# Kernel tuning notes

Measured on AMD Instinct MI355X. Metric: run time of the kernel, lower is better.

The kernel has to match this reference:

```python
import jax, jax.numpy as jnp
import numpy as np

B = 256      # batch
ZD = 128     # z_dim
HIN = 128    # H_inputs
H = 512      # hidden
HT = 32      # H_t
N = 16384    # num nodes
RW = 16      # rw_len
TEMP = 1.0
P_DROP = 0.2
EPS_C = 0.1  # constraints epsilon


def setup_inputs() -> dict:
    key = jax.random.key(0)
    ks = jax.random.split(key, 20)
    def w(k, shape, fan):
        return (jax.random.normal(k, shape, jnp.float32) / np.float32(np.sqrt(fan)))
    z = lambda n: jnp.zeros((n,), jnp.float32)
    u = jax.random.uniform(ks[14], (RW, B, N), jnp.float32)
    return {
        "latent": jax.random.normal(ks[0], (B, ZD + 1), jnp.float32),
        "inputs0": jnp.zeros((B, HIN), jnp.float32),
        "Wc": w(ks[1], (ZD, ZD + 1), ZD + 1), "bc": z(ZD),
        "Ws": w(ks[2], (H, ZD), ZD), "bs": z(H),
        "Wh": w(ks[3], (H, H), H), "bh": z(H),
        "Wcc": w(ks[4], (H, H), H), "bcc": z(H),
        "W_ih": w(ks[5], (4 * H, HIN), HIN), "b_ih": z(4 * H),
        "W_hh": w(ks[6], (4 * H, H), H), "b_hh": z(4 * H),
        "W_up": w(ks[7], (N, H), H), "b_up": z(N),
        "W_down": w(ks[8], (HIN, N), N),
        "Wt_down": w(ks[9], (HT, H), H), "bt_down": z(HT),
        "Wt_pred": w(ks[10], (1, HT), HT),
        "Wt_up": w(ks[11], (HT, 1), 1), "bt_up": z(HT),
        "W_vt": w(ks[12], (HIN, HIN + HT), HIN + HT),
        "W_prob": w(ks[13], (1, HIN), HIN),
        # pre-sampled Gumbel noise per step (torch.rand -> gumbel)
        "gumbel": -jnp.log(-jnp.log(u + 1e-20) + 1e-20),
        # uniforms for dropout masks in TimeDecoder (forced train mode)
        "drop_u": jax.random.uniform(ks[15], (RW, B, HT), jnp.float32),
    }


def reference(latent, inputs0, Wc, bc, Ws, bs, Wh, bh, Wcc, bcc,
              W_ih, b_ih, W_hh, b_hh, W_up, b_up, W_down,
              Wt_down, bt_down, Wt_pred, Wt_up, bt_up, W_vt, W_prob,
              gumbel, drop_u):
    # induced=True path: compress latent, init (h, c)
    lat = jnp.tanh(latent @ Wc.T + bc)               # [B, ZD]
    s = jnp.tanh(lat @ Ws.T + bs)                    # [B, H]
    h0 = jnp.tanh(s @ Wh.T + bh)
    c0 = jnp.tanh(s @ Wcc.T + bcc)
    keep = 1.0 - P_DROP

    def step(carry, xs):
        x, h, c, last_t = carry
        g, du = xs
        # torch LSTMCell: gate order i, f, g, o
        gates = x @ W_ih.T + b_ih + h @ W_hh.T + b_hh  # [B, 4H]
        i, f, gg, o = jnp.split(gates, 4, axis=1)
        c2 = jax.nn.sigmoid(f) * c + jax.nn.sigmoid(i) * jnp.tanh(gg)
        h2 = jax.nn.sigmoid(o) * jnp.tanh(c2)
        # node logits + gumbel-softmax sample
        p = h2 @ W_up.T + b_up                         # [B, N]
        v = jax.nn.softmax((p + g) / TEMP, axis=1)
        Hg = v @ W_down.T                              # [B, HIN]
        # TimeDecoder (dropout always in train mode)
        td = jnp.tanh(h2 @ Wt_down.T + bt_down)        # [B, HT]
        td = td * (du < keep).astype(td.dtype) / keep
        t = jnp.minimum(td @ Wt_pred.T, 1.0)           # [B, 1]
        # constraints(t, last_t)
        mn = jnp.min(t)
        t = jnp.where(mn < EPS_C, t - mn, t)
        mx = jnp.max(t)
        t = jnp.where(mx > 1.0, t / mx, t)
        t = jnp.clip(t, last_t, 1.0)
        Ht = t @ Wt_up.T + bt_up                       # [B, HT]
        x2 = jnp.concatenate([Hg, Ht], axis=1) @ W_vt.T  # [B, HIN]
        return (x2, h2, c2, t), (v, t)

    last_t0 = jnp.zeros((latent.shape[0], 1), latent.dtype)
    (xf, _, _, _), (rw, ts) = jax.lax.scan(step, (inputs0, h0, c0, last_t0), (gumbel, drop_u))
    rw = jnp.transpose(rw, (1, 0, 2))   # [B, RW, N]
    ts = jnp.transpose(ts, (1, 0, 2))   # [B, RW, 1]
    prob = xf @ W_prob.T                # [B, 1]
    return rw, ts, prob
```

## Files before the change

### kernel.cpp

```cpp
#include <hip/hip_runtime.h>

typedef float  __attribute__((ext_vector_type(4))) f32x4;
typedef int    __attribute__((ext_vector_type(4))) i32x4;
typedef unsigned short u16;
typedef unsigned long long u64;

#define B    256
#define H    512
#define HIN  128
#define N    16384
#define RW   16
#define HT   32
#define KC2  672
#define RWN  262144
#define TS_OFF   67108864
#define PROB_OFF 67112960

__device__ __forceinline__ u16 f2bf(float f) {
  unsigned u = __builtin_bit_cast(unsigned, f);
  u += 0x7FFFu + ((u >> 16) & 1u);
  return (u16)(u >> 16);
}
__device__ __forceinline__ float bf2f(u16 v) {
  return __builtin_bit_cast(float, ((unsigned)v) << 16);
}
__device__ __forceinline__ float sigm(float x) { return 1.0f / (1.0f + expf(-x)); }

__device__ __forceinline__ void mfma(f32x4& d, i32x4 a, i32x4 b) {
  asm volatile("v_mfma_f32_16x16x32_bf16 %0, %1, %2, %0" : "+v"(d) : "v"(a), "v"(b));
}
__device__ __forceinline__ void mfma_n(f32x4& d, i32x4 a, i32x4 b) {
  asm volatile("s_nop 1\n\tv_mfma_f32_16x16x32_bf16 %0, %1, %2, %0" : "+v"(d) : "v"(a), "v"(b));
}
__device__ __forceinline__ void fence_acc(f32x4& v) {
  asm volatile("s_nop 7\n\ts_nop 7" : "+v"(v));
}

__global__ __launch_bounds__(256) void k_prep(
    const float* __restrict__ W_up, const float* __restrict__ W_down,
    const float* __restrict__ W_hh, const float* __restrict__ Wt_down,
    const float* __restrict__ b_ih, const float* __restrict__ b_hh,
    const float* __restrict__ Wh, const float* __restrict__ Wcc,
    u16* __restrict__ Wup_b, u16* __restrict__ Wdn_b, u16* __restrict__ Wfull,
    u16* __restrict__ Wtd_b, u16* __restrict__ Whc_b,
    float* __restrict__ bcomb, float* __restrict__ tstep, float* __restrict__ rowLs)
{
  const int idx0 = blockIdx.x * 256 + threadIdx.x;
  const int stride = gridDim.x * 256;
  for (int i = idx0; i < N * H; i += stride) Wup_b[i] = f2bf(W_up[i]);
  for (int i = idx0; i < HIN * N; i += stride) Wdn_b[i] = f2bf(W_down[i]);
  for (int i = idx0; i < 4 * H * H; i += stride) {
    int j = i >> 9, k = i & 511;
    Wfull[j * KC2 + 160 + k] = f2bf(W_hh[i]);
  }
  for (int i = idx0; i < HT * H; i += stride) Wtd_b[i] = f2bf(Wt_down[i]);
  for (int i = idx0; i < 2 * H * H; i += stride) {
    int j = i >> 9, k = i & 511;
    Whc_b[i] = f2bf(j < H ? Wh[j * H + k] : Wcc[(j - H) * H + k]);
  }
  for (int i = idx0; i < 4 * H; i += stride) bcomb[i] = b_ih[i] + b_hh[i];
  for (int i = idx0; i < B; i += stride) tstep[i] = 0.0f;
  for (int i = idx0; i < 16 * B; i += stride) rowLs[i] = 0.0f;
}

__global__ __launch_bounds__(256) void k_fold(
    const float* __restrict__ W_ih, const float* __restrict__ W_vt,
    const float* __restrict__ inputs0, const float* __restrict__ W_prob,
    u16* __restrict__ Wfull, float* __restrict__ g0add, float* __restrict__ wpc)
{
  int idx = blockIdx.x * 256 + threadIdx.x;
  if (idx < 2048 * 160) {
    int j = idx / 160, m = idx - j * 160;
    float a = 0.0f;
    for (int c = 0; c < HIN; ++c) a += W_ih[j * HIN + c] * W_vt[c * 160 + m];
    Wfull[j * KC2 + m] = f2bf(a);
  } else if (idx < 2048 * 160 + 256 * 2048) {
    int i2 = idx - 2048 * 160;
    int b = i2 >> 11, j = i2 & 2047;
    float a = 0.0f;
    for (int k = 0; k < HIN; ++k) a += inputs0[b * HIN + k] * W_ih[j * HIN + k];
    g0add[i2] = a;
  } else if (idx < 2048 * 160 + 256 * 2048 + 160) {
    int m = idx - (2048 * 160 + 256 * 2048);
    float a = 0.0f;
    for (int k = 0; k < HIN; ++k) a += W_prob[k] * W_vt[k * 160 + m];
    wpc[m] = a;
  }
}

__global__ __launch_bounds__(256) void k_lat(
    const float* __restrict__ latent, const float* __restrict__ Wc,
    const float* __restrict__ bc, float* __restrict__ latbuf)
{
  int idx = blockIdx.x * 256 + threadIdx.x;
  int b = idx >> 7, i = idx & 127;
  float acc = bc[i];
  for (int k = 0; k < 129; ++k) acc += latent[b * 129 + k] * Wc[i * 129 + k];
  latbuf[idx] = tanhf(acc);
}

__global__ __launch_bounds__(256) void k_sinit(
    const float* __restrict__ latbuf, const float* __restrict__ Ws,
    const float* __restrict__ bs, u16* __restrict__ sinit_b)
{
  int idx = blockIdx.x * 256 + threadIdx.x;
  int b = idx >> 9, j = idx & 511;
  float acc = bs[j];
  for (int k = 0; k < HIN; ++k) acc += latbuf[b * HIN + k] * Ws[j * HIN + k];
  sinit_b[idx] = f2bf(tanhf(acc));
}

__global__ __launch_bounds__(256) void k_h0c0m(
    const u16* __restrict__ sinit_b, const u16* __restrict__ Whc_b,
    const float* __restrict__ bh, const float* __restrict__ bcc,
    float* __restrict__ cbuf, u16* __restrict__ h0out)
{
  const int rb = blockIdx.x >> 6, cb = blockIdx.x & 63;
  const int wave = threadIdx.x >> 6, lane = threadIdx.x & 63;
  const int lr = lane & 15, lk = lane >> 4;
  const int m0 = rb * 16, col0 = cb * 16;
  const u16* ab = sinit_b + (m0 + lr) * H + wave * 128 + 8 * lk;
  const u16* bb = Whc_b + (col0 + lr) * H + wave * 128 + 8 * lk;
  f32x4 acc[2] = {};
  mfma_n(acc[0], *(const i32x4*)(ab),      *(const i32x4*)(bb));
  mfma_n(acc[1], *(const i32x4*)(ab + 32), *(const i32x4*)(bb + 32));
  mfma(acc[0], *(const i32x4*)(ab + 64), *(const i32x4*)(bb + 64));
  mfma(acc[1], *(const i32x4*)(ab + 96), *(const i32x4*)(bb + 96));
  fence_acc(acc[0]); fence_acc(acc[1]);
  __shared__ float q[4][16][17];
  #pragma unroll
  for (int rr = 0; rr < 4; ++rr)
    q[wave][4 * lk + rr][lr] = acc[0][rr] + acc[1][rr];
  __syncthreads();
  const int r2 = threadIdx.x >> 4, jj = threadIdx.x & 15;
  float s = q[0][r2][jj] + q[1][r2][jj] + q[2][r2][jj] + q[3][r2][jj];
  int col = col0 + jj;
  if (col < H) h0out[(m0 + r2) * H + col] = f2bf(tanhf(s + bh[col]));
  else         cbuf[(m0 + r2) * H + col - H] = tanhf(s + bcc[col - H]);
}

__global__ __launch_bounds__(256) void k_lstm2(
    const u16* __restrict__ hprev, u16* __restrict__ hcur,
    const u16* __restrict__ Wfull, const float* __restrict__ bcomb,
    float* __restrict__ cbuf, const float* __restrict__ g0,
    const float* __restrict__ HgfPrev, float* __restrict__ HgfNext,
    const float* __restrict__ rowLs, const float* __restrict__ t0buf,
    float* __restrict__ tstep, const float* __restrict__ Wt_up,
    const float* __restrict__ bt_up, float* __restrict__ out,
    const u16* __restrict__ ebp, int r)
{
  const int blk = blockIdx.x, tid = threadIdx.x;
  const int wave = tid >> 6, lane = tid & 63;
  const int lr = lane & 15, lk = lane >> 4;
  const int rb = blk & 15, cb = blk >> 4;
  const int m0 = rb * 16, j0 = cb * 16;
  const float* rowLprev = rowLs + (r - 1) * B;

  __shared__ u16 aT[16][168];
  __shared__ float q[4][16][17];
  __shared__ float redS[8];
  __shared__ float tl[256];

  if (blk < 128) HgfNext[blk * 256 + tid] = 0.0f;

  float tv = 0.0f;
  if (r > 0) {
    tv = t0buf[tid];
    float v = tv;
    #pragma unroll
    for (int off = 1; off < 64; off <<= 1) v = fminf(v, __shfl_xor(v, off));
    if (lane == 0) redS[wave] = v;
  }
  __syncthreads();
  if (r > 0) {
    float mn = fminf(fminf(redS[0], redS[1]), fminf(redS[2], redS[3]));
    if (mn < 0.1f) tv -= mn;
    float v = tv;
    #pragma unroll
    for (int off = 1; off < 64; off <<= 1) v = fmaxf(v, __shfl_xor(v, off));
    if (lane == 0) redS[4 + wave] = v;
  }
  __syncthreads();
  if (r > 0) {
    float mx = fmaxf(fmaxf(redS[4], redS[5]), fmaxf(redS[6], redS[7]));
    if (mx > 1.0f) tv /= mx;
    tv = fminf(fmaxf(tv, tstep[(r - 1) * B + tid]), 1.0f);
    if (blk == 0) {
      tstep[r * B + tid] = tv;
      out[TS_OFF + tid * RW + (r - 1)] = tv;
    }
  }
  tl[tid] = tv;

  {
    const int row = tid >> 4, c8 = (tid & 15) * 8;
    if (r > 0) {
      const float* hp = HgfPrev + (m0 + row) * HIN + c8;
      f32x4 x0 = *(const f32x4*)hp;
      f32x4 x1 = *(const f32x4*)(hp + 4);
      float R = 1.0f / rowLprev[m0 + row];
      aT[row][c8 + 0] = f2bf(x0[0] * R); aT[row][c8 + 1] = f2bf(x0[1] * R);
      aT[row][c8 + 2] = f2bf(x0[2] * R); aT[row][c8 + 3] = f2bf(x0[3] * R);
      aT[row][c8 + 4] = f2bf(x1[0] * R); aT[row][c8 + 5] = f2bf(x1[1] * R);
      aT[row][c8 + 6] = f2bf(x1[2] * R); aT[row][c8 + 7] = f2bf(x1[3] * R);
    } else {
      #pragma unroll
      for (int e = 0; e < 8; ++e) aT[row][c8 + e] = 0;
    }
  }

  __syncthreads();
  for (int i2 = tid; i2 < 512; i2 += 256) {
    int row = i2 >> 5, j = i2 & 31;
    aT[row][128 + j] = (r > 0) ? f2bf(tl[m0 + row] * Wt_up[j] + bt_up[j]) : (u16)0;
  }

  if (r > 0) {
    #pragma unroll
    for (int uu = 0; uu < 8; ++uu) {
      int flat = (blk * 2048 + uu * 256 + tid) * 4;
      int row = flat >> 14;
      float Rv = 1.0f / rowLprev[row];
      u64 ev = *(const u64*)(ebp + flat);
      f32x4 o;
      o[0] = bf2f((u16)ev) * Rv;
      o[1] = bf2f((u16)(ev >> 16)) * Rv;
      o[2] = bf2f((u16)(ev >> 32)) * Rv;
      o[3] = bf2f((u16)(ev >> 48)) * Rv;
      *(f32x4*)(out + (size_t)row * RWN + (size_t)(r - 1) * N + (flat & (N - 1))) = o;
    }
  }
  __syncthreads();

  const int gcol = wave * H + j0 + lr;
  f32x4 acc[2] = {};
  const u16* brow = Wfull + (size_t)gcol * KC2 + 8 * lk;
  const u16* aL   = &aT[lr][8 * lk];
  const u16* arow = hprev + (m0 + lr) * H + 8 * lk;
  mfma_n(acc[0], *(const i32x4*)(aL),       *(const i32x4*)(brow));
  mfma_n(acc[1], *(const i32x4*)(aL + 32),  *(const i32x4*)(brow + 32));
  mfma(acc[0], *(const i32x4*)(aL + 64),  *(const i32x4*)(brow + 64));
  mfma(acc[1], *(const i32x4*)(aL + 96),  *(const i32x4*)(brow + 96));
  mfma(acc[0], *(const i32x4*)(aL + 128), *(const i32x4*)(brow + 128));
  #pragma unroll 4
  for (int i = 5; i < 21; ++i) {
    int kk = i * 32;
    mfma(acc[i & 1], *(const i32x4*)(arow + kk - 160), *(const i32x4*)(brow + kk));
  }
  fence_acc(acc[0]); fence_acc(acc[1]);
  float bias = bcomb[gcol];
  #pragma unroll
  for (int rr = 0; rr < 4; ++rr)
    q[wave][4 * lk + rr][lr] = acc[0][rr] + acc[1][rr] + bias;
  __syncthreads();
  const int r2 = tid >> 4, jj = tid & 15;
  const int b = m0 + r2, j = j0 + jj;
  float gi = q[0][r2][jj], gf = q[1][r2][jj], gg = q[2][r2][jj], go = q[3][r2][jj];
  if (r == 0) {
    const float* gp = g0 + b * 2048 + j;
    gi += gp[0]; gf += gp[512]; gg += gp[1024]; go += gp[1536];
  }
  float c  = cbuf[b * H + j];
  float c2 = sigm(gf) * c + sigm(gi) * tanhf(gg);
  float h2 = sigm(go) * tanhf(c2);
  cbuf[b * H + j] = c2;
  hcur[b * H + j] = f2bf(h2);
}

__global__ __launch_bounds__(256) void k_pgemm2(
    const u16* __restrict__ hb, const u16* __restrict__ Wup,
    const float* __restrict__ b_up, const float* __restrict__ gum,
    u16* __restrict__ eb, float* __restrict__ rowL,
    float* __restrict__ HgfAcc, const u16* __restrict__ Wdn,
    const u16* __restrict__ Wtd, const float* __restrict__ bt_down,
    const float* __restrict__ Wt_pred, const float* __restrict__ du,
    float* __restrict__ t0)
{
  const int rb = blockIdx.x >> 7, cb = blockIdx.x & 127;
  const int wave = threadIdx.x >> 6, lane = threadIdx.x & 63;
  const int lr = lane & 15, lk = lane >> 4;
  const int m0 = rb * 32;
  const int n0 = cb * 128 + wave * 32;

  float gv[2][4][2], bup0 = b_up[n0 + lr], bup1 = b_up[n0 + 16 + lr];
  #pragma unroll
  for (int mi = 0; mi < 2; ++mi)
    #pragma unroll
    for (int rr = 0; rr < 4; ++rr) {
      int row = m0 + 16 * mi + 4 * lk + rr;
      gv[mi][rr][0] = gum[(size_t)row * N + n0 + lr];
      gv[mi][rr][1] = gum[(size_t)row * N + n0 + 16 + lr];
    }

  f32x4 acc[2][2] = {};
  const u16* a0 = hb + (m0 + lr) * H + 8 * lk;
  const u16* a1 = a0 + 16 * H;
  const u16* b0 = Wup + (size_t)(n0 + lr) * H + 8 * lk;
  const u16* b1 = b0 + 16 * H;
  {
    i32x4 af0 = *(const i32x4*)(a0);
    i32x4 af1 = *(const i32x4*)(a1);
    i32x4 bf0 = *(const i32x4*)(b0);
    i32x4 bf1 = *(const i32x4*)(b1);
    mfma_n(acc[0][0], af0, bf0); mfma_n(acc[0][1], af0, bf1);
    mfma_n(acc[1][0], af1, bf0); mfma_n(acc[1][1], af1, bf1);
  }
  #pragma unroll 3
  for (int kk = 32; kk < H; kk += 32) {
    i32x4 af0 = *(const i32x4*)(a0 + kk);
    i32x4 af1 = *(const i32x4*)(a1 + kk);
    i32x4 bf0 = *(const i32x4*)(b0 + kk);
    i32x4 bf1 = *(const i32x4*)(b1 + kk);
    mfma(acc[0][0], af0, bf0); mfma(acc[0][1], af0, bf1);
    mfma(acc[1][0], af1, bf0); mfma(acc[1][1], af1, bf1);
  }
  #pragma unroll
  for (int mi = 0; mi < 2; ++mi) { fence_acc(acc[mi][0]); fence_acc(acc[mi][1]); }

  __shared__ float eL[32][132];
  __shared__ float sL[4][32];
  #pragma unroll
  for (int mi = 0; mi < 2; ++mi)
    #pragma unroll
    for (int rr = 0; rr < 4; ++rr) {
      int rl = 16 * mi + 4 * lk + rr;
      int row = m0 + rl;
      u16* sp = eb + (size_t)row * N + n0 + lr;
      float v0 = acc[mi][0][rr] + bup0 + gv[mi][rr][0];
      float v1 = acc[mi][1][rr] + bup1 + gv[mi][rr][1];
      float e0 = expf(fminf(v0, 80.0f));
      float e1 = expf(fminf(v1, 80.0f));
      sp[0] = f2bf(e0); sp[16] = f2bf(e1);
      eL[rl][wave * 32 + lr] = e0;
      eL[rl][wave * 32 + 16 + lr] = e1;
      float par = e0 + e1;
      #pragma unroll
      for (int off = 1; off < 16; off <<= 1) par += __shfl_xor(par, off);
      if (lr == 0) sL[wave][rl] = par;
    }
  __syncthreads();
  if (threadIdx.x < 32)
    atomicAdd(rowL + m0 + threadIdx.x,
              sL[0][threadIdx.x] + sL[1][threadIdx.x] + sL[2][threadIdx.x] + sL[3][threadIdx.x]);

  const int nb = cb * 128;
  f32x4 acc2[2][2] = {};
  #pragma unroll
  for (int kk2 = 0; kk2 < 4; ++kk2) {
    i32x4 af[2];
    #pragma unroll
    for (int mi2 = 0; mi2 < 2; ++mi2) {
      const float* ep = &eL[16 * mi2 + lr][kk2 * 32 + 8 * lk];
      f32x4 x0 = *(const f32x4*)ep;
      f32x4 x1 = *(const f32x4*)(ep + 4);
      af[mi2][0] = (int)f2bf(x0[0]) | ((int)f2bf(x0[1]) << 16);
      af[mi2][1] = (int)f2bf(x0[2]) | ((int)f2bf(x0[3]) << 16);
      af[mi2][2] = (int)f2bf(x1[0]) | ((int)f2bf(x1[1]) << 16);
      af[mi2][3] = (int)f2bf(x1[2]) | ((int)f2bf(x1[3]) << 16);
    }
    i32x4 bf0 = *(const i32x4*)(Wdn + (size_t)(wave * 32 + lr) * N + nb + kk2 * 32 + 8 * lk);
    i32x4 bf1 = *(const i32x4*)(Wdn + (size_t)(wave * 32 + 16 + lr) * N + nb + kk2 * 32 + 8 * lk);
    mfma_n(acc2[0][0], af[0], bf0); mfma_n(acc2[0][1], af[0], bf1);
    mfma_n(acc2[1][0], af[1], bf0); mfma_n(acc2[1][1], af[1], bf1);
  }
  #pragma unroll
  for (int mi2 = 0; mi2 < 2; ++mi2) { fence_acc(acc2[mi2][0]); fence_acc(acc2[mi2][1]); }
  #pragma unroll
  for (int mi2 = 0; mi2 < 2; ++mi2)
    #pragma unroll
    for (int ni = 0; ni < 2; ++ni)
      #pragma unroll
      for (int rr = 0; rr < 4; ++rr)
        atomicAdd(HgfAcc + (m0 + 16 * mi2 + 4 * lk + rr) * HIN + wave * 32 + 16 * ni + lr,
                  acc2[mi2][ni][rr]);

  if (cb == 0 && wave < 2) {
    f32x4 acc3[2] = {};
    const u16* at = hb + (m0 + wave * 16 + lr) * H + 8 * lk;
    {
      i32x4 af = *(const i32x4*)(at);
      mfma_n(acc3[0], af, *(const i32x4*)(Wtd + lr * H + 8 * lk));
      mfma_n(acc3[1], af, *(const i32x4*)(Wtd + (16 + lr) * H + 8 * lk));
    }
    for (int kk = 32; kk < H; kk += 32) {
      i32x4 af = *(const i32x4*)(at + kk);
      mfma(acc3[0], af, *(const i32x4*)(Wtd + lr * H + kk + 8 * lk));
      mfma(acc3[1], af, *(const i32x4*)(Wtd + (16 + lr) * H + kk + 8 * lk));
    }
    fence_acc(acc3[0]); fence_acc(acc3[1]);
    float wp0 = Wt_pred[lr],  wp1 = Wt_pred[16 + lr];
    float bt0 = bt_down[lr],  bt1 = bt_down[16 + lr];
    #pragma unroll
    for (int rr = 0; rr < 4; ++rr) {
      int row = m0 + wave * 16 + 4 * lk + rr;
      float td0 = tanhf(acc3[0][rr] + bt0);
      float td1 = tanhf(acc3[1][rr] + bt1);
      td0 = (du[row * HT + lr]      < 0.8f) ? td0 * 1.25f : 0.0f;
      td1 = (du[row * HT + 16 + lr] < 0.8f) ? td1 * 1.25f : 0.0f;
      float part = td0 * wp0 + td1 * wp1;
      #pragma unroll
      for (int off = 1; off < 16; off <<= 1) part += __shfl_xor(part, off);
      if (lr == 0) t0[row] = fminf(part, 1.0f);
    }
  }
}

__global__ __launch_bounds__(256) void k_tail(
    float* __restrict__ out, const u16* __restrict__ eb15,
    const float* __restrict__ rowLs, const float* __restrict__ t0buf,
    float* __restrict__ tstep)
{
  const int blk = blockIdx.x, tid = threadIdx.x;
  const float* rowL15 = rowLs + 15 * B;
  #pragma unroll
  for (int uu = 0; uu < 4; ++uu) {
    int flat = (blk * 1024 + uu * 256 + tid) * 4;
    int row = flat >> 14;
    float Rv = 1.0f / rowL15[row];
    u64 ev = *(const u64*)(eb15 + flat);
    f32x4 o;
    o[0] = bf2f((u16)ev) * Rv;
    o[1] = bf2f((u16)(ev >> 16)) * Rv;
    o[2] = bf2f((u16)(ev >> 32)) * Rv;
    o[3] = bf2f((u16)(ev >> 48)) * Rv;
    *(f32x4*)(out + (size_t)row * RWN + (size_t)15 * N + (flat & (N - 1))) = o;
  }
  if (blk == 0) {
    const int wave = tid >> 6, lane = tid & 63;
    __shared__ float redS[8];
    float tv = t0buf[tid];
    float v = tv;
    #pragma unroll
    for (int off = 1; off < 64; off <<= 1) v = fminf(v, __shfl_xor(v, off));
    if (lane == 0) redS[wave] = v;
    __syncthreads();
    float mn = fminf(fminf(redS[0], redS[1]), fminf(redS[2], redS[3]));
    if (mn < 0.1f) tv -= mn;
    v = tv;
    #pragma unroll
    for (int off = 1; off < 64; off <<= 1) v = fmaxf(v, __shfl_xor(v, off));
    if (lane == 0) redS[4 + wave] = v;
    __syncthreads();
    float mx = fmaxf(fmaxf(redS[4], redS[5]), fmaxf(redS[6], redS[7]));
    if (mx > 1.0f) tv /= mx;
    tv = fminf(fmaxf(tv, tstep[15 * B + tid]), 1.0f);
    tstep[16 * B + tid] = tv;
    out[TS_OFF + tid * RW + 15] = tv;
  }
}

__global__ __launch_bounds__(256) void k_prob(
    const float* __restrict__ Hgf15, const float* __restrict__ rowLs,
    const float* __restrict__ tstep, const float* __restrict__ Wt_up,
    const float* __restrict__ bt_up, const float* __restrict__ wpc,
    float* __restrict__ outp)
{
  int b = threadIdx.x;
  float R = 1.0f / rowLs[15 * B + b];
  float acc = 0.0f;
  for (int m = 0; m < HIN; ++m) acc += Hgf15[b * HIN + m] * R * wpc[m];
  float tv = tstep[16 * B + b];
  for (int j = 0; j < HT; ++j) acc += (tv * Wt_up[j] + bt_up[j]) * wpc[HIN + j];
  outp[b] = acc;
}

extern "C" void kernel_launch(void* const* d_in, const int* in_sizes, int n_in,
                              void* d_out, int out_size, void* d_ws, size_t ws_size,
                              hipStream_t stream) {
  (void)in_sizes; (void)n_in; (void)out_size; (void)ws_size;
  const float* latent  = (const float*)d_in[0];
  const float* inputs0 = (const float*)d_in[1];
  const float* Wc      = (const float*)d_in[2];
  const float* bc      = (const float*)d_in[3];
  const float* Ws      = (const float*)d_in[4];
  const float* bs      = (const float*)d_in[5];
  const float* Wh      = (const float*)d_in[6];
  const float* bh      = (const float*)d_in[7];
  const float* Wcc     = (const float*)d_in[8];
  const float* bcc     = (const float*)d_in[9];
  const float* W_ih    = (const float*)d_in[10];
  const float* b_ih    = (const float*)d_in[11];
  const float* W_hh    = (const float*)d_in[12];
  const float* b_hh    = (const float*)d_in[13];
  const float* W_up    = (const float*)d_in[14];
  const float* b_up    = (const float*)d_in[15];
  const float* W_down  = (const float*)d_in[16];
  const float* Wt_down = (const float*)d_in[17];
  const float* bt_down = (const float*)d_in[18];
  const float* Wt_pred = (const float*)d_in[19];
  const float* Wt_up   = (const float*)d_in[20];
  const float* bt_up   = (const float*)d_in[21];
  const float* W_vt    = (const float*)d_in[22];
  const float* W_prob  = (const float*)d_in[23];
  const float* gumbel  = (const float*)d_in[24];
  const float* drop_u  = (const float*)d_in[25];
  float* out = (float*)d_out;

  char* p = (char*)d_ws;
  auto alloc = [&](size_t bytes) { char* r = p; p += (bytes + 255) & ~(size_t)255; return r; };
  u16*   Wup_b  = (u16*)  alloc((size_t)N * H * 2);
  u16*   Wdn_b  = (u16*)  alloc((size_t)HIN * N * 2);
  u16*   Wfull_b= (u16*)  alloc((size_t)4 * H * KC2 * 2);
  u16*   Wtd_b  = (u16*)  alloc((size_t)HT * H * 2);
  u16*   Whc_b  = (u16*)  alloc((size_t)2 * H * H * 2);
  float* bcomb  = (float*)alloc(4 * H * 4);
  u16*   hbuf0  = (u16*)  alloc((size_t)B * H * 2);
  u16*   hbuf1  = (u16*)  alloc((size_t)B * H * 2);
  float* cbuf   = (float*)alloc((size_t)B * H * 4);
  u16*   sinit_b= (u16*)  alloc((size_t)B * H * 2);
  float* latbuf = (float*)alloc((size_t)B * HIN * 4);
  float* rowLs  = (float*)alloc((size_t)16 * B * 4);
  float* t0buf  = (float*)alloc(B * 4);
  float* tstep  = (float*)alloc((size_t)17 * B * 4);
  float* Hgf2_0 = (float*)alloc((size_t)B * HIN * 4);
  float* Hgf2_1 = (float*)alloc((size_t)B * HIN * 4);
  float* g0add  = (float*)alloc((size_t)B * 4 * H * 4);
  float* wpc    = (float*)alloc(160 * 4);
  u16*   ebuf0  = (u16*)  alloc((size_t)B * N * 2);
  u16*   ebuf1  = (u16*)  alloc((size_t)B * N * 2);

  k_prep<<<2048, 256, 0, stream>>>(W_up, W_down, W_hh, Wt_down, b_ih, b_hh, Wh, Wcc,
                                   Wup_b, Wdn_b, Wfull_b, Wtd_b, Whc_b, bcomb,
                                   tstep, rowLs);
  k_fold<<<3330, 256, 0, stream>>>(W_ih, W_vt, inputs0, W_prob, Wfull_b, g0add, wpc);
  k_lat  <<<128, 256, 0, stream>>>(latent, Wc, bc, latbuf);
  k_sinit<<<512, 256, 0, stream>>>(latbuf, Ws, bs, sinit_b);
  k_h0c0m<<<1024, 256, 0, stream>>>(sinit_b, Whc_b, bh, bcc, cbuf, hbuf1);

  for (int r = 0; r < 16; ++r) {
    u16* hprev = (r & 1) ? hbuf0 : hbuf1;
    u16* hcur  = (r & 1) ? hbuf1 : hbuf0;
    u16* eb    = (r & 1) ? ebuf1 : ebuf0;
    u16* ebp   = (r & 1) ? ebuf0 : ebuf1;
    float* HgfCur  = (r & 1) ? Hgf2_1 : Hgf2_0;
    float* HgfPrev = (r & 1) ? Hgf2_0 : Hgf2_1;
    k_lstm2<<<512, 256, 0, stream>>>(hprev, hcur, Wfull_b, bcomb, cbuf, g0add,
                                     HgfPrev, HgfCur, rowLs, t0buf, tstep,
                                     Wt_up, bt_up, out, ebp, r);
    k_pgemm2<<<1024, 256, 0, stream>>>(hcur, Wup_b, b_up, gumbel + (size_t)r * B * N,
                                       eb, rowLs + r * B, HgfCur, Wdn_b,
                                       Wtd_b, bt_down, Wt_pred,
                                       drop_u + (size_t)r * B * HT, t0buf);
  }
  k_tail<<<1024, 256, 0, stream>>>(out, ebuf1, rowLs, t0buf, tstep);
  k_prob<<<1, 256, 0, stream>>>(Hgf2_1, rowLs, tstep, Wt_up, bt_up, wpc, out + PROB_OFF);
}
```

Before: 1.293 ms.

## Move rw output writeback into pgemm, split Hg atomics, fuse small kernels

The normalized rw output writeback for the previous step moves out of the latency-bound LSTM kernel into the wide pgemm kernel, where it can overlap with the GEMM. The Hg accumulator is split into 8 partial slices to reduce atomic contention, and consumers sum the slices. The exp values are staged in LDS as bf16 instead of fp32, which removes the repacking before the second MFMA, and the s_nop padding on those MFMAs is dropped. k_fold is merged into k_prep and k_prob into k_tail to save launches, at the cost of a serialized grid-stride fold and more buffer memory.

```diff
diff --git a/kernel.cpp b/kernel.cpp
--- a/kernel.cpp
+++ b/kernel.cpp
@@ -41,9 +41,12 @@
     const float* __restrict__ W_hh, const float* __restrict__ Wt_down,
     const float* __restrict__ b_ih, const float* __restrict__ b_hh,
     const float* __restrict__ Wh, const float* __restrict__ Wcc,
+    const float* __restrict__ W_ih, const float* __restrict__ W_vt,
+    const float* __restrict__ inputs0, const float* __restrict__ W_prob,
     u16* __restrict__ Wup_b, u16* __restrict__ Wdn_b, u16* __restrict__ Wfull,
     u16* __restrict__ Wtd_b, u16* __restrict__ Whc_b,
-    float* __restrict__ bcomb, float* __restrict__ tstep, float* __restrict__ rowLs)
+    float* __restrict__ bcomb, float* __restrict__ tstep, float* __restrict__ rowLs,
+    float* __restrict__ g0add, float* __restrict__ wpc)
 {
   const int idx0 = blockIdx.x * 256 + threadIdx.x;
   const int stride = gridDim.x * 256;
@@ -61,30 +64,22 @@
   for (int i = idx0; i < 4 * H; i += stride) bcomb[i] = b_ih[i] + b_hh[i];
   for (int i = idx0; i < B; i += stride) tstep[i] = 0.0f;
   for (int i = idx0; i < 16 * B; i += stride) rowLs[i] = 0.0f;
-}
-
-__global__ __launch_bounds__(256) void k_fold(
-    const float* __restrict__ W_ih, const float* __restrict__ W_vt,
-    const float* __restrict__ inputs0, const float* __restrict__ W_prob,
-    u16* __restrict__ Wfull, float* __restrict__ g0add, float* __restrict__ wpc)
-{
-  int idx = blockIdx.x * 256 + threadIdx.x;
-  if (idx < 2048 * 160) {
-    int j = idx / 160, m = idx - j * 160;
+  for (int i = idx0; i < 2048 * 160; i += stride) {
+    int j = i / 160, m = i - j * 160;
     float a = 0.0f;
     for (int c = 0; c < HIN; ++c) a += W_ih[j * HIN + c] * W_vt[c * 160 + m];
     Wfull[j * KC2 + m] = f2bf(a);
-  } else if (idx < 2048 * 160 + 256 * 2048) {
-    int i2 = idx - 2048 * 160;
-    int b = i2 >> 11, j = i2 & 2047;
+  }
+  for (int i = idx0; i < 256 * 2048; i += stride) {
+    int b = i >> 11, j = i & 2047;
     float a = 0.0f;
     for (int k = 0; k < HIN; ++k) a += inputs0[b * HIN + k] * W_ih[j * HIN + k];
-    g0add[i2] = a;
-  } else if (idx < 2048 * 160 + 256 * 2048 + 160) {
-    int m = idx - (2048 * 160 + 256 * 2048);
+    g0add[i] = a;
+  }
+  for (int i = idx0; i < 160; i += stride) {
     float a = 0.0f;
-    for (int k = 0; k < HIN; ++k) a += W_prob[k] * W_vt[k * 160 + m];
-    wpc[m] = a;
+    for (int k = 0; k < HIN; ++k) a += W_prob[k] * W_vt[k * 160 + i];
+    wpc[i] = a;
   }
 }
 
@@ -143,11 +138,10 @@
     const u16* __restrict__ hprev, u16* __restrict__ hcur,
     const u16* __restrict__ Wfull, const float* __restrict__ bcomb,
     float* __restrict__ cbuf, const float* __restrict__ g0,
-    const float* __restrict__ HgfPrev, float* __restrict__ HgfNext,
+    const float* __restrict__ HgXprev, float* __restrict__ HgXcur,
     const float* __restrict__ rowLs, const float* __restrict__ t0buf,
     float* __restrict__ tstep, const float* __restrict__ Wt_up,
-    const float* __restrict__ bt_up, float* __restrict__ out,
-    const u16* __restrict__ ebp, int r)
+    const float* __restrict__ bt_up, float* __restrict__ out, int r)
 {
   const int blk = blockIdx.x, tid = threadIdx.x;
   const int wave = tid >> 6, lane = tid & 63;
@@ -161,7 +155,8 @@
   __shared__ float redS[8];
   __shared__ float tl[256];
 
-  if (blk < 128) HgfNext[blk * 256 + tid] = 0.0f;
+  HgXcur[blk * 512 + tid] = 0.0f;
+  HgXcur[blk * 512 + 256 + tid] = 0.0f;
 
   float tv = 0.0f;
   if (r > 0) {
@@ -195,40 +190,28 @@
   {
     const int row = tid >> 4, c8 = (tid & 15) * 8;
     if (r > 0) {
-      const float* hp = HgfPrev + (m0 + row) * HIN + c8;
-      f32x4 x0 = *(const f32x4*)hp;
-      f32x4 x1 = *(const f32x4*)(hp + 4);
+      const float* hp = HgXprev + (size_t)(m0 + row) * HIN + c8;
+      f32x4 A0 = {}, A1 = {};
+      #pragma unroll
+      for (int x = 0; x < 8; ++x) {
+        A0 += *(const f32x4*)(hp + (size_t)x * (B * HIN));
+        A1 += *(const f32x4*)(hp + (size_t)x * (B * HIN) + 4);
+      }
       float R = 1.0f / rowLprev[m0 + row];
-      aT[row][c8 + 0] = f2bf(x0[0] * R); aT[row][c8 + 1] = f2bf(x0[1] * R);
-      aT[row][c8 + 2] = f2bf(x0[2] * R); aT[row][c8 + 3] = f2bf(x0[3] * R);
-      aT[row][c8 + 4] = f2bf(x1[0] * R); aT[row][c8 + 5] = f2bf(x1[1] * R);
-      aT[row][c8 + 6] = f2bf(x1[2] * R); aT[row][c8 + 7] = f2bf(x1[3] * R);
+      aT[row][c8 + 0] = f2bf(A0[0] * R); aT[row][c8 + 1] = f2bf(A0[1] * R);
+      aT[row][c8 + 2] = f2bf(A0[2] * R); aT[row][c8 + 3] = f2bf(A0[3] * R);
+      aT[row][c8 + 4] = f2bf(A1[0] * R); aT[row][c8 + 5] = f2bf(A1[1] * R);
+      aT[row][c8 + 6] = f2bf(A1[2] * R); aT[row][c8 + 7] = f2bf(A1[3] * R);
     } else {
       #pragma unroll
       for (int e = 0; e < 8; ++e) aT[row][c8 + e] = 0;
     }
   }
-
-  __syncthreads();
+  __syncthreads();
+
   for (int i2 = tid; i2 < 512; i2 += 256) {
     int row = i2 >> 5, j = i2 & 31;
     aT[row][128 + j] = (r > 0) ? f2bf(tl[m0 + row] * Wt_up[j] + bt_up[j]) : (u16)0;
-  }
-
-  if (r > 0) {
-    #pragma unroll
-    for (int uu = 0; uu < 8; ++uu) {
-      int flat = (blk * 2048 + uu * 256 + tid) * 4;
-      int row = flat >> 14;
-      float Rv = 1.0f / rowLprev[row];
-      u64 ev = *(const u64*)(ebp + flat);
-      f32x4 o;
-      o[0] = bf2f((u16)ev) * Rv;
-      o[1] = bf2f((u16)(ev >> 16)) * Rv;
-      o[2] = bf2f((u16)(ev >> 32)) * Rv;
-      o[3] = bf2f((u16)(ev >> 48)) * Rv;
-      *(f32x4*)(out + (size_t)row * RWN + (size_t)(r - 1) * N + (flat & (N - 1))) = o;
-    }
   }
   __syncthreads();
 
@@ -270,13 +253,15 @@
 __global__ __launch_bounds__(256) void k_pgemm2(
     const u16* __restrict__ hb, const u16* __restrict__ Wup,
     const float* __restrict__ b_up, const float* __restrict__ gum,
-    u16* __restrict__ eb, float* __restrict__ rowL,
-    float* __restrict__ HgfAcc, const u16* __restrict__ Wdn,
+    u16* __restrict__ eb, const u16* __restrict__ ebp,
+    float* __restrict__ rowL, const float* __restrict__ rowLs,
+    float* __restrict__ HgX, const u16* __restrict__ Wdn,
     const u16* __restrict__ Wtd, const float* __restrict__ bt_down,
     const float* __restrict__ Wt_pred, const float* __restrict__ du,
-    float* __restrict__ t0)
-{
-  const int rb = blockIdx.x >> 7, cb = blockIdx.x & 127;
+    float* __restrict__ t0, float* __restrict__ out, int r)
+{
+  const int blk = blockIdx.x;
+  const int rb = blk >> 7, cb = blk & 127;
   const int wave = threadIdx.x >> 6, lane = threadIdx.x & 63;
   const int lr = lane & 15, lk = lane >> 4;
   const int m0 = rb * 32;
@@ -291,6 +276,23 @@
       gv[mi][rr][0] = gum[(size_t)row * N + n0 + lr];
       gv[mi][rr][1] = gum[(size_t)row * N + n0 + 16 + lr];
     }
+
+  if (r > 0) {
+    const float* rowLprev = rowLs + (r - 1) * B;
+    #pragma unroll
+    for (int uu = 0; uu < 4; ++uu) {
+      int flat = (blk * 1024 + uu * 256 + (int)threadIdx.x) * 4;
+      int row = flat >> 14;
+      float Rv = 1.0f / rowLprev[row];
+      u64 ev = *(const u64*)(ebp + flat);
+      f32x4 o;
+      o[0] = bf2f((u16)ev) * Rv;
+      o[1] = bf2f((u16)(ev >> 16)) * Rv;
+      o[2] = bf2f((u16)(ev >> 32)) * Rv;
+      o[3] = bf2f((u16)(ev >> 48)) * Rv;
+      *(f32x4*)(out + (size_t)row * RWN + (size_t)(r - 1) * N + (flat & (N - 1))) = o;
+    }
+  }
 
   f32x4 acc[2][2] = {};
   const u16* a0 = hb + (m0 + lr) * H + 8 * lk;
@@ -317,7 +319,7 @@
   #pragma unroll
   for (int mi = 0; mi < 2; ++mi) { fence_acc(acc[mi][0]); fence_acc(acc[mi][1]); }
 
-  __shared__ float eL[32][132];
+  __shared__ u16 eLb[32][136];
   __shared__ float sL[4][32];
   #pragma unroll
   for (int mi = 0; mi < 2; ++mi)
@@ -330,9 +332,10 @@
       float v1 = acc[mi][1][rr] + bup1 + gv[mi][rr][1];
       float e0 = expf(fminf(v0, 80.0f));
       float e1 = expf(fminf(v1, 80.0f));
-      sp[0] = f2bf(e0); sp[16] = f2bf(e1);
-      eL[rl][wave * 32 + lr] = e0;
-      eL[rl][wave * 32 + 16 + lr] = e1;
+      u16 p0 = f2bf(e0), p1 = f2bf(e1);
+      sp[0] = p0; sp[16] = p1;
+      eLb[rl][wave * 32 + lr] = p0;
+      eLb[rl][wave * 32 + 16 + lr] = p1;
       float par = e0 + e1;
       #pragma unroll
       for (int off = 1; off < 16; off <<= 1) par += __shfl_xor(par, off);
@@ -344,24 +347,16 @@
               sL[0][threadIdx.x] + sL[1][threadIdx.x] + sL[2][threadIdx.x] + sL[3][threadIdx.x]);
 
   const int nb = cb * 128;
+  float* hgs = HgX + (size_t)(blk & 7) * (B * HIN);
   f32x4 acc2[2][2] = {};
   #pragma unroll
   for (int kk2 = 0; kk2 < 4; ++kk2) {
-    i32x4 af[2];
-    #pragma unroll
-    for (int mi2 = 0; mi2 < 2; ++mi2) {
-      const float* ep = &eL[16 * mi2 + lr][kk2 * 32 + 8 * lk];
-      f32x4 x0 = *(const f32x4*)ep;
-      f32x4 x1 = *(const f32x4*)(ep + 4);
-      af[mi2][0] = (int)f2bf(x0[0]) | ((int)f2bf(x0[1]) << 16);
-      af[mi2][1] = (int)f2bf(x0[2]) | ((int)f2bf(x0[3]) << 16);
-      af[mi2][2] = (int)f2bf(x1[0]) | ((int)f2bf(x1[1]) << 16);
-      af[mi2][3] = (int)f2bf(x1[2]) | ((int)f2bf(x1[3]) << 16);
-    }
+    i32x4 af0 = *(const i32x4*)(&eLb[lr][kk2 * 32 + 8 * lk]);
+    i32x4 af1 = *(const i32x4*)(&eLb[16 + lr][kk2 * 32 + 8 * lk]);
     i32x4 bf0 = *(const i32x4*)(Wdn + (size_t)(wave * 32 + lr) * N + nb + kk2 * 32 + 8 * lk);
     i32x4 bf1 = *(const i32x4*)(Wdn + (size_t)(wave * 32 + 16 + lr) * N + nb + kk2 * 32 + 8 * lk);
-    mfma_n(acc2[0][0], af[0], bf0); mfma_n(acc2[0][1], af[0], bf1);
-    mfma_n(acc2[1][0], af[1], bf0); mfma_n(acc2[1][1], af[1], bf1);
+    mfma(acc2[0][0], af0, bf0); mfma(acc2[0][1], af0, bf1);
+    mfma(acc2[1][0], af1, bf0); mfma(acc2[1][1], af1, bf1);
   }
   #pragma unroll
   for (int mi2 = 0; mi2 < 2; ++mi2) { fence_acc(acc2[mi2][0]); fence_acc(acc2[mi2][1]); }
@@ -371,7 +366,7 @@
     for (int ni = 0; ni < 2; ++ni)
       #pragma unroll
       for (int rr = 0; rr < 4; ++rr)
-        atomicAdd(HgfAcc + (m0 + 16 * mi2 + 4 * lk + rr) * HIN + wave * 32 + 16 * ni + lr,
+        atomicAdd(hgs + (m0 + 16 * mi2 + 4 * lk + rr) * HIN + wave * 32 + 16 * ni + lr,
                   acc2[mi2][ni][rr]);
 
   if (cb == 0 && wave < 2) {
@@ -408,24 +403,28 @@
 __global__ __launch_bounds__(256) void k_tail(
     float* __restrict__ out, const u16* __restrict__ eb15,
     const float* __restrict__ rowLs, const float* __restrict__ t0buf,
-    float* __restrict__ tstep)
+    float* __restrict__ tstep, const float* __restrict__ HgX15,
+    const float* __restrict__ Wt_up, const float* __restrict__ bt_up,
+    const float* __restrict__ wpc)
 {
   const int blk = blockIdx.x, tid = threadIdx.x;
   const float* rowL15 = rowLs + 15 * B;
-  #pragma unroll
-  for (int uu = 0; uu < 4; ++uu) {
-    int flat = (blk * 1024 + uu * 256 + tid) * 4;
-    int row = flat >> 14;
-    float Rv = 1.0f / rowL15[row];
-    u64 ev = *(const u64*)(eb15 + flat);
-    f32x4 o;
-    o[0] = bf2f((u16)ev) * Rv;
-    o[1] = bf2f((u16)(ev >> 16)) * Rv;
-    o[2] = bf2f((u16)(ev >> 32)) * Rv;
-    o[3] = bf2f((u16)(ev >> 48)) * Rv;
-    *(f32x4*)(out + (size_t)row * RWN + (size_t)15 * N + (flat & (N - 1))) = o;
-  }
-  if (blk == 0) {
+  if (blk < 1024) {
+    #pragma unroll
+    for (int uu = 0; uu < 4; ++uu) {
+      int flat = (blk * 1024 + uu * 256 + tid) * 4;
+      int row = flat >> 14;
+      float Rv = 1.0f / rowL15[row];
+      u64 ev = *(const u64*)(eb15 + flat);
+      f32x4 o;
+      o[0] = bf2f((u16)ev) * Rv;
+      o[1] = bf2f((u16)(ev >> 16)) * Rv;
+      o[2] = bf2f((u16)(ev >> 32)) * Rv;
+      o[3] = bf2f((u16)(ev >> 48)) * Rv;
+      *(f32x4*)(out + (size_t)row * RWN + (size_t)15 * N + (flat & (N - 1))) = o;
+    }
+  }
+  if (blk == 0 || blk == 1024) {
     const int wave = tid >> 6, lane = tid & 63;
     __shared__ float redS[8];
     float tv = t0buf[tid];
@@ -444,24 +443,20 @@
     float mx = fmaxf(fmaxf(redS[4], redS[5]), fmaxf(redS[6], redS[7]));
     if (mx > 1.0f) tv /= mx;
     tv = fminf(fmaxf(tv, tstep[15 * B + tid]), 1.0f);
-    tstep[16 * B + tid] = tv;
-    out[TS_OFF + tid * RW + 15] = tv;
-  }
-}
-
-__global__ __launch_bounds__(256) void k_prob(
-    const float* __restrict__ Hgf15, const float* __restrict__ rowLs,
-    const float* __restrict__ tstep, const float* __restrict__ Wt_up,
-    const float* __restrict__ bt_up, const float* __restrict__ wpc,
-    float* __restrict__ outp)
-{
-  int b = threadIdx.x;
-  float R = 1.0f / rowLs[15 * B + b];
-  float acc = 0.0f;
-  for (int m = 0; m < HIN; ++m) acc += Hgf15[b * HIN + m] * R * wpc[m];
-  float tv = tstep[16 * B + b];
-  for (int j = 0; j < HT; ++j) acc += (tv * Wt_up[j] + bt_up[j]) * wpc[HIN + j];
-  outp[b] = acc;
+    if (blk == 0) out[TS_OFF + tid * RW + 15] = tv;
+    else {
+      float R = 1.0f / rowL15[tid];
+      float acc = 0.0f;
+      for (int m = 0; m < HIN; ++m) {
+        float hg = 0.0f;
+        #pragma unroll
+        for (int x = 0; x < 8; ++x) hg += HgX15[(size_t)x * (B * HIN) + tid * HIN + m];
+        acc += hg * R * wpc[m];
+      }
+      for (int j = 0; j < HT; ++j) acc += (tv * Wt_up[j] + bt_up[j]) * wpc[HIN + j];
+      out[PROB_OFF + tid] = acc;
+    }
+  }
 }
 
 extern "C" void kernel_launch(void* const* d_in, const int* in_sizes, int n_in,
@@ -512,17 +507,17 @@
   float* rowLs  = (float*)alloc((size_t)16 * B * 4);
   float* t0buf  = (float*)alloc(B * 4);
   float* tstep  = (float*)alloc((size_t)17 * B * 4);
-  float* Hgf2_0 = (float*)alloc((size_t)B * HIN * 4);
-  float* Hgf2_1 = (float*)alloc((size_t)B * HIN * 4);
+  float* HgX0   = (float*)alloc((size_t)8 * B * HIN * 4);
+  float* HgX1   = (float*)alloc((size_t)8 * B * HIN * 4);
   float* g0add  = (float*)alloc((size_t)B * 4 * H * 4);
   float* wpc    = (float*)alloc(160 * 4);
   u16*   ebuf0  = (u16*)  alloc((size_t)B * N * 2);
   u16*   ebuf1  = (u16*)  alloc((size_t)B * N * 2);
 
   k_prep<<<2048, 256, 0, stream>>>(W_up, W_down, W_hh, Wt_down, b_ih, b_hh, Wh, Wcc,
+                                   W_ih, W_vt, inputs0, W_prob,
                                    Wup_b, Wdn_b, Wfull_b, Wtd_b, Whc_b, bcomb,
-                                   tstep, rowLs);
-  k_fold<<<3330, 256, 0, stream>>>(W_ih, W_vt, inputs0, W_prob, Wfull_b, g0add, wpc);
+                                   tstep, rowLs, g0add, wpc);
   k_lat  <<<128, 256, 0, stream>>>(latent, Wc, bc, latbuf);
   k_sinit<<<512, 256, 0, stream>>>(latbuf, Ws, bs, sinit_b);
   k_h0c0m<<<1024, 256, 0, stream>>>(sinit_b, Whc_b, bh, bcc, cbuf, hbuf1);
@@ -532,16 +527,16 @@
     u16* hcur  = (r & 1) ? hbuf1 : hbuf0;
     u16* eb    = (r & 1) ? ebuf1 : ebuf0;
     u16* ebp   = (r & 1) ? ebuf0 : ebuf1;
-    float* HgfCur  = (r & 1) ? Hgf2_1 : Hgf2_0;
-    float* HgfPrev = (r & 1) ? Hgf2_0 : Hgf2_1;
+    float* HgXc = (r & 1) ? HgX1 : HgX0;
+    float* HgXp = (r & 1) ? HgX0 : HgX1;
     k_lstm2<<<512, 256, 0, stream>>>(hprev, hcur, Wfull_b, bcomb, cbuf, g0add,
-                                     HgfPrev, HgfCur, rowLs, t0buf, tstep,
-                                     Wt_up, bt_up, out, ebp, r);
+                                     HgXp, HgXc, rowLs, t0buf, tstep,
+                                     Wt_up, bt_up, out, r);
     k_pgemm2<<<1024, 256, 0, stream>>>(hcur, Wup_b, b_up, gumbel + (size_t)r * B * N,
-                                       eb, rowLs + r * B, HgfCur, Wdn_b,
+                                       eb, ebp, rowLs + r * B, rowLs, HgXc, Wdn_b,
                                        Wtd_b, bt_down, Wt_pred,
-                                       drop_u + (size_t)r * B * HT, t0buf);
-  }
-  k_tail<<<1024, 256, 0, stream>>>(out, ebuf1, rowLs, t0buf, tstep);
-  k_prob<<<1, 256, 0, stream>>>(Hgf2_1, rowLs, tstep, Wt_up, bt_up, wpc, out + PROB_OFF);
-}
+                                       drop_u + (size_t)r * B * HT, t0buf, out, r);
+  }
+  k_tail<<<1025, 256, 0, stream>>>(out, ebuf1, rowLs, t0buf, tstep, HgX1,
+                                   Wt_up, bt_up, wpc);
+}
```

Result: slower. 1.354 ms (+4.7%).
